# Kernel optimization log

Hardware: AMD Instinct MI355X
Metric: run time of the kernel (lower is better)

## Reference

```python
import jax, jax.numpy as jnp
import numpy as np

NS, NT, DIN, DOUT = 4096, 8192, 256, 128


def setup_inputs() -> dict:
    key = jax.random.key(0)
    k1, k2, k3, k4, k5, k6 = jax.random.split(key, 6)
    inp_s = jax.random.normal(k1, (NS, DIN), dtype=jnp.float32)
    inp_t = jax.random.normal(k2, (NT, DIN), dtype=jnp.float32)
    # nonnegative adjacency weights (original graphs have 0/1 entries)
    adj = jax.random.uniform(k3, (NS, NT), dtype=jnp.float32)
    adj_s = jax.random.uniform(k4, (NS, NS), dtype=jnp.float32)
    adj_t = jax.random.uniform(k5, (NT, NT), dtype=jnp.float32)
    init_range = np.sqrt(6.0 / (DIN + DOUT))
    W = jax.random.uniform(k6, (DIN, DOUT), minval=-init_range, maxval=init_range,
                           dtype=jnp.float32)
    return {"inp_s": inp_s, "inp_t": inp_t, "adj": adj, "adj_s": adj_s,
            "adj_t": adj_t, "W": W}


def reference(inp_s, inp_t, adj, adj_s, adj_t, W):
    # project both node sets with shared weights (dropout = 0.0)
    x = inp_s @ W                                   # [Ns, Dout]
    y = inp_t @ W                                   # [Nt, Dout]

    # degree normalization (add-one before sqrt)
    deg_so = jnp.sum(adj, axis=1, keepdims=True) + jnp.sum(adj_s, axis=1, keepdims=True)  # [Ns,1]
    root_deg_so = jnp.sqrt(deg_so + 1.0)            # [Ns,1]
    deg_to = jnp.sum(adj, axis=0, keepdims=True) + jnp.sum(adj_t, axis=0, keepdims=True)  # [1,Nt]
    root_deg_to = jnp.sqrt(deg_to + 1.0)            # [1,Nt]

    nrm_adj_s = adj_s / root_deg_so / root_deg_so.T  # [Ns,Ns]
    nrm_adj_t = adj_t / root_deg_to / root_deg_to.T  # [Nt,Nt]
    nrm_adj = adj / root_deg_so / root_deg_to        # [Ns,Nt]

    x = jax.nn.relu(x / root_deg_so + nrm_adj_s @ x + nrm_adj @ y)
    # note: updated (activated) x feeds into y's cross term, as in the original
    y = jax.nn.relu(y / root_deg_to.T + nrm_adj_t @ y + nrm_adj.T @ x)
    return (x, y)
```

## Files before the change

### kernel.cpp

```cpp
#include <hip/hip_runtime.h>

#define NS 4096
#define NT 8192
#define DIN 256
#define DOUT 128

#define OFF_RS   0
#define OFF_RT   (NS)
#define OFF_C1   (OFF_RT + NT)
#define OFF_C2   (OFF_C1 + NS*DOUT)
#define OFF_XS   (OFF_C2 + NT*DOUT)
#define OFF_YS   (OFF_XS + NS*DOUT)
#define OFF_XNS  (OFF_YS + NT*DOUT)
#define OFF_XST  (OFF_XNS + NS*DOUT)
#define OFF_YST  (OFF_XST + (128*NS)/2)

typedef __attribute__((ext_vector_type(8))) short bf8v;
typedef __attribute__((ext_vector_type(4))) float f32x4;
typedef __attribute__((ext_vector_type(4))) unsigned short u16x4;

__device__ __forceinline__ ushort f2bf(float f) {
    unsigned x = __float_as_uint(f);
    unsigned r = (x + 0x7fffu + ((x >> 16) & 1u)) >> 16;
    return (ushort)r;
}

__global__ void zero_kernel(float* __restrict__ p, int n4) {
    int i = blockIdx.x * blockDim.x + threadIdx.x;
    int stride = gridDim.x * blockDim.x;
    float4* p4 = (float4*)p;
    float4 z = make_float4(0.f, 0.f, 0.f, 0.f);
    for (; i < n4; i += stride) p4[i] = z;
}

__global__ __launch_bounds__(256)
void deg_mega_kernel(const float* __restrict__ adj,
                     const float* __restrict__ adj_s,
                     const float* __restrict__ adj_t,
                     float* __restrict__ deg_s, float* __restrict__ deg_t) {
    const int tid = threadIdx.x;
    const int lane = tid & 63;
    const int bid = blockIdx.x;
    if (bid < 1024) {
        const int c4 = (bid & 7) * 256 + tid;
        const int r0 = (bid >> 3) * 64;
        const float4* A4 = (const float4*)adj_t + (size_t)r0 * (NT / 4) + c4;
        float sx = 0.f, sy = 0.f, sz = 0.f, sw = 0.f;
#pragma unroll 8
        for (int r = 0; r < 64; ++r) {
            float4 v = A4[(size_t)r * (NT / 4)];
            sx += v.x; sy += v.y; sz += v.z; sw += v.w;
        }
        float* d = deg_t + c4 * 4;
        unsafeAtomicAdd(d + 0, sx);
        unsafeAtomicAdd(d + 1, sy);
        unsafeAtomicAdd(d + 2, sz);
        unsafeAtomicAdd(d + 3, sw);
    } else if (bid < 2048) {
        const int b = bid - 1024;
        const int c4 = (b & 7) * 256 + tid;
        const int r0 = (b >> 3) * 32;
        const float4* A4 = (const float4*)adj + (size_t)r0 * (NT / 4) + c4;
        float sx = 0.f, sy = 0.f, sz = 0.f, sw = 0.f;
#pragma unroll 8
        for (int r = 0; r < 32; ++r) {
            float4 v = A4[(size_t)r * (NT / 4)];
            sx += v.x; sy += v.y; sz += v.z; sw += v.w;
            float rp = v.x + v.y + v.z + v.w;
#pragma unroll
            for (int off = 32; off > 0; off >>= 1) rp += __shfl_down(rp, off, 64);
            if (lane == 0) unsafeAtomicAdd(deg_s + r0 + r, rp);
        }
        float* d = deg_t + c4 * 4;
        unsafeAtomicAdd(d + 0, sx);
        unsafeAtomicAdd(d + 1, sy);
        unsafeAtomicAdd(d + 2, sz);
        unsafeAtomicAdd(d + 3, sw);
    } else {
        const int b = bid - 2048;
        const int wid = tid >> 6;
        const int row = b * 4 + wid;
        const float4* p = (const float4*)(adj_s + (size_t)row * NS);
        float sum = 0.f;
#pragma unroll 8
        for (int c = lane; c < NS / 4; c += 64) { float4 v = p[c]; sum += v.x + v.y + v.z + v.w; }
#pragma unroll
        for (int off = 32; off > 0; off >>= 1) sum += __shfl_down(sum, off, 64);
        if (lane == 0) unsafeAtomicAdd(deg_s + row, sum);
    }
}

__global__ void finish_deg_kernel(float* __restrict__ deg) {
    int t = blockIdx.x * blockDim.x + threadIdx.x;
    deg[t] = sqrtf(deg[t] + 1.0f);
}

__global__ __launch_bounds__(256)
void proj_scale_kernel(const float* __restrict__ inp_s,
                       const float* __restrict__ inp_t,
                       const float* __restrict__ W,
                       const float* __restrict__ rs, const float* __restrict__ rt,
                       float* __restrict__ xs, float* __restrict__ ys,
                       ushort* __restrict__ xsT, ushort* __restrict__ ysT) {
    __shared__ float As[32][68];
    __shared__ float Bs[32][128];
    const int tid = threadIdx.x;

    const float* inp; const float* rdeg; float* outp; ushort* outT; int M; int m0;
    if (blockIdx.x < NS / 64) {
        inp = inp_s; rdeg = rs; outp = xs; outT = xsT; M = NS; m0 = blockIdx.x * 64;
    } else {
        int b = blockIdx.x - NS / 64;
        inp = inp_t; rdeg = rt; outp = ys; outT = ysT; M = NT; m0 = b * 64;
    }

    const int tx = tid & 15, ty = tid >> 4;
    const int arow = tid >> 3, acg = tid & 7;
    const int bk = tid >> 5, bng = tid & 31;

    float acc[4][8];
#pragma unroll
    for (int r = 0; r < 4; ++r)
#pragma unroll
        for (int c = 0; c < 8; ++c) acc[r][c] = 0.f;

    for (int kt = 0; kt < DIN; kt += 32) {
        const float* Ab = inp + (size_t)(m0 + arow) * DIN + kt + acg * 4;
        float4 a0 = *(const float4*)Ab;
        float4 a1 = *(const float4*)(Ab + (size_t)32 * DIN);
        const float* Bb = W + (size_t)(kt + bk) * DOUT + bng * 4;
        float4 b0 = *(const float4*)Bb;
        float4 b1 = *(const float4*)(Bb + 8 * DOUT);
        float4 b2 = *(const float4*)(Bb + 16 * DOUT);
        float4 b3 = *(const float4*)(Bb + 24 * DOUT);
        __syncthreads();
        As[acg * 4 + 0][arow] = a0.x;
        As[acg * 4 + 1][arow] = a0.y;
        As[acg * 4 + 2][arow] = a0.z;
        As[acg * 4 + 3][arow] = a0.w;
        As[acg * 4 + 0][arow + 32] = a1.x;
        As[acg * 4 + 1][arow + 32] = a1.y;
        As[acg * 4 + 2][arow + 32] = a1.z;
        As[acg * 4 + 3][arow + 32] = a1.w;
        *(float4*)&Bs[bk][bng * 4] = b0;
        *(float4*)&Bs[bk + 8][bng * 4] = b1;
        *(float4*)&Bs[bk + 16][bng * 4] = b2;
        *(float4*)&Bs[bk + 24][bng * 4] = b3;
        __syncthreads();
#pragma unroll
        for (int k = 0; k < 32; ++k) {
            float4 av = *(const float4*)&As[k][ty * 4];
            float4 bv0 = *(const float4*)&Bs[k][tx * 4];
            float4 bv1 = *(const float4*)&Bs[k][tx * 4 + 64];
            float a[4] = {av.x, av.y, av.z, av.w};
            float b[8] = {bv0.x, bv0.y, bv0.z, bv0.w, bv1.x, bv1.y, bv1.z, bv1.w};
#pragma unroll
            for (int r = 0; r < 4; ++r)
#pragma unroll
                for (int c = 0; c < 8; ++c) acc[r][c] = fmaf(a[r], b[c], acc[r][c]);
        }
    }
    float rds[4];
#pragma unroll
    for (int r = 0; r < 4; ++r) rds[r] = rdeg[m0 + ty * 4 + r];
#pragma unroll
    for (int r = 0; r < 4; ++r) {
        int row = m0 + ty * 4 + r;
        float* orow = outp + (size_t)row * DOUT;
#pragma unroll
        for (int c = 0; c < 8; ++c) acc[r][c] /= rds[r];
#pragma unroll
        for (int c = 0; c < 4; ++c) {
            orow[tx * 4 + c] = acc[r][c];
            orow[tx * 4 + 64 + c] = acc[r][4 + c];
        }
    }
#pragma unroll
    for (int c = 0; c < 8; ++c) {
        int col = tx * 4 + (c & 3) + (c >> 2) * 64;
        u16x4 w;
#pragma unroll
        for (int r = 0; r < 4; ++r) w[r] = f2bf(acc[r][c]);
        *(u16x4*)&outT[(size_t)col * M + m0 + ty * 4] = w;
    }
}

template<int TRANS, int BTF>
__device__ __forceinline__
void gemm_body(ushort (*As)[40], ushort (*Bs)[40],
               const float* __restrict__ A, int lda,
               const float* __restrict__ Bf,
               const ushort* __restrict__ bT, int ldb,
               float* __restrict__ C, int kchunk, int k0, int m0) {
    const int tid = threadIdx.x;
    const int lane = tid & 63, wid = tid >> 6;
    const int wm = (wid >> 1) * 64, wn = (wid & 1) * 64;
    const int r16 = lane & 15, kg = lane >> 4;

    const int s_kr = tid >> 3, s_f4 = tid & 7;
    const int a_r = tid >> 1, a_seg = tid & 1;
    const int t_n = tid >> 2, t_seg = tid & 3;

    f32x4 acc[4][4];
#pragma unroll
    for (int i = 0; i < 4; ++i)
#pragma unroll
        for (int j = 0; j < 4; ++j) acc[i][j] = (f32x4)(0.f);

    float4 aP[4], bP[4];
    bf8v bPT[2];

    auto loadB = [&](int ktb) {
        if (BTF) {
            const ushort* Tb = bT + (size_t)t_n * ldb + k0 + ktb + t_seg * 8;
            bPT[0] = *(const bf8v*)Tb;
            bPT[1] = *(const bf8v*)(Tb + (size_t)64 * ldb);
        } else {
            const float* Bb = Bf + (size_t)(k0 + ktb + s_kr) * DOUT + s_f4 * 4;
#pragma unroll
            for (int i = 0; i < 4; ++i) bP[i] = *(const float4*)(Bb + i * 32);
        }
    };
    auto loadA = [&](int ktb) {
        if (TRANS) {
            const float* Ab = A + (size_t)(k0 + ktb + s_kr) * lda + m0 + s_f4 * 4;
#pragma unroll
            for (int i = 0; i < 4; ++i) aP[i] = *(const float4*)(Ab + i * 32);
        } else {
            const float* Ab = A + (size_t)(m0 + a_r) * lda + k0 + ktb + a_seg * 16;
#pragma unroll
            for (int i = 0; i < 4; ++i) aP[i] = *(const float4*)(Ab + i * 4);
        }
    };

    loadB(0); loadA(0);

    for (int kt = 0; kt < kchunk; kt += 32) {
        __syncthreads();
        if (TRANS) {
#pragma unroll
            for (int i = 0; i < 4; ++i) {
                int m = s_f4 * 4 + i * 32;
                As[m + 0][s_kr] = f2bf(aP[i].x);
                As[m + 1][s_kr] = f2bf(aP[i].y);
                As[m + 2][s_kr] = f2bf(aP[i].z);
                As[m + 3][s_kr] = f2bf(aP[i].w);
            }
        } else {
            bf8v w0, w1;
            w0[0] = (short)f2bf(aP[0].x); w0[1] = (short)f2bf(aP[0].y);
            w0[2] = (short)f2bf(aP[0].z); w0[3] = (short)f2bf(aP[0].w);
            w0[4] = (short)f2bf(aP[1].x); w0[5] = (short)f2bf(aP[1].y);
            w0[6] = (short)f2bf(aP[1].z); w0[7] = (short)f2bf(aP[1].w);
            w1[0] = (short)f2bf(aP[2].x); w1[1] = (short)f2bf(aP[2].y);
            w1[2] = (short)f2bf(aP[2].z); w1[3] = (short)f2bf(aP[2].w);
            w1[4] = (short)f2bf(aP[3].x); w1[5] = (short)f2bf(aP[3].y);
            w1[6] = (short)f2bf(aP[3].z); w1[7] = (short)f2bf(aP[3].w);
            *(bf8v*)&As[a_r][a_seg * 16] = w0;
            *(bf8v*)&As[a_r][a_seg * 16 + 8] = w1;
        }
        if (BTF) {
            *(bf8v*)&Bs[t_n][t_seg * 8] = bPT[0];
            *(bf8v*)&Bs[t_n + 64][t_seg * 8] = bPT[1];
        } else {
#pragma unroll
            for (int i = 0; i < 4; ++i) {
                int n = s_f4 * 4 + i * 32;
                Bs[n + 0][s_kr] = f2bf(bP[i].x);
                Bs[n + 1][s_kr] = f2bf(bP[i].y);
                Bs[n + 2][s_kr] = f2bf(bP[i].z);
                Bs[n + 3][s_kr] = f2bf(bP[i].w);
            }
        }
        __syncthreads();

        if (kt + 32 < kchunk) { loadB(kt + 32); loadA(kt + 32); }

        bf8v af[4], bfv[4];
#pragma unroll
        for (int f = 0; f < 4; ++f) af[f] = *(const bf8v*)&As[wm + f * 16 + r16][kg * 8];
#pragma unroll
        for (int f = 0; f < 4; ++f) bfv[f] = *(const bf8v*)&Bs[wn + f * 16 + r16][kg * 8];
#pragma unroll
        for (int i = 0; i < 4; ++i)
#pragma unroll
            for (int j = 0; j < 4; ++j)
                acc[i][j] = __builtin_amdgcn_mfma_f32_16x16x32_bf16(af[i], bfv[j], acc[i][j], 0, 0, 0);
    }

    const int crow0 = m0 + wm + (lane >> 4) * 4;
#pragma unroll
    for (int i = 0; i < 4; ++i) {
#pragma unroll
        for (int j = 0; j < 4; ++j) {
            float* base = C + (size_t)(crow0 + i * 16) * DOUT + wn + j * 16 + r16;
            unsafeAtomicAdd(base + 0 * DOUT, acc[i][j][0]);
            unsafeAtomicAdd(base + 1 * DOUT, acc[i][j][1]);
            unsafeAtomicAdd(base + 2 * DOUT, acc[i][j][2]);
            unsafeAtomicAdd(base + 3 * DOUT, acc[i][j][3]);
        }
    }
}

__global__ __launch_bounds__(256)
void gemm_triple_kernel(const float* __restrict__ A0, int lda0, const ushort* __restrict__ B0T, int ldb0, int kc0, int n0,
                        const float* __restrict__ A1, int lda1, const ushort* __restrict__ B1T, int ldb1, int kc1, int n1,
                        const float* __restrict__ A2, int lda2, const ushort* __restrict__ B2T, int ldb2, int kc2,
                        float* __restrict__ C0, float* __restrict__ C2) {
    __shared__ ushort As[128][40];
    __shared__ ushort Bs[128][40];
    int bid = blockIdx.x;
    if (bid < n0) {
        gemm_body<0, 1>(As, Bs, A0, lda0, nullptr, B0T, ldb0, C0, kc0, (bid & 7) * kc0, (bid >> 3) * 128);
    } else if (bid < n0 + n1) {
        int b = bid - n0;
        gemm_body<0, 1>(As, Bs, A1, lda1, nullptr, B1T, ldb1, C0, kc1, (b & 7) * kc1, (b >> 3) * 128);
    } else {
        int b = bid - n0 - n1;
        gemm_body<0, 1>(As, Bs, A2, lda2, nullptr, B2T, ldb2, C2, kc2, (b & 7) * kc2, (b >> 3) * 128);
    }
}

template<int TRANS, int BTF>
__global__ __launch_bounds__(256)
void gemm_single_kernel(const float* __restrict__ A, int lda,
                        const float* __restrict__ Bf, const ushort* __restrict__ bT, int ldb,
                        float* __restrict__ C, int kchunk) {
    __shared__ ushort As[128][40];
    __shared__ ushort Bs[128][40];
    gemm_body<TRANS, BTF>(As, Bs, A, lda, Bf, bT, ldb, C, kchunk, blockIdx.y * kchunk, blockIdx.x * 128);
}

__global__ void epilogue1_kernel(const float* __restrict__ C1,
                                 const float* __restrict__ xs,
                                 const float* __restrict__ rs,
                                 float* __restrict__ outx,
                                 float* __restrict__ xns) {
    int idx = blockIdx.x * blockDim.x + threadIdx.x;
    if (idx >= NS * DOUT) return;
    int row = idx >> 7;
    float r = rs[row];
    float v = xs[idx] + C1[idx] / r;
    v = v > 0.f ? v : 0.f;
    outx[idx] = v;
    xns[idx] = v / r;
}

__global__ void epilogue2_kernel(const float* __restrict__ C2,
                                 const float* __restrict__ ys,
                                 const float* __restrict__ rt,
                                 float* __restrict__ outy) {
    int idx = blockIdx.x * blockDim.x + threadIdx.x;
    if (idx >= NT * DOUT) return;
    int row = idx >> 7;
    float v = ys[idx] + C2[idx] / rt[row];
    v = v > 0.f ? v : 0.f;
    outy[idx] = v;
}

extern "C" void kernel_launch(void* const* d_in, const int* in_sizes, int n_in,
                              void* d_out, int out_size, void* d_ws, size_t ws_size,
                              hipStream_t stream) {
    const float* inp_s = (const float*)d_in[0];
    const float* inp_t = (const float*)d_in[1];
    const float* adj   = (const float*)d_in[2];
    const float* adj_s = (const float*)d_in[3];
    const float* adj_t = (const float*)d_in[4];
    const float* W     = (const float*)d_in[5];
    float* out = (float*)d_out;
    float* ws  = (float*)d_ws;

    float* rs  = ws + OFF_RS;
    float* rt  = ws + OFF_RT;
    float* C1  = ws + OFF_C1;
    float* C2  = ws + OFF_C2;
    float* xs  = ws + OFF_XS;
    float* ys  = ws + OFF_YS;
    float* xns = ws + OFF_XNS;
    ushort* xsT = (ushort*)(ws + OFF_XST);
    ushort* ysT = (ushort*)(ws + OFF_YST);

    zero_kernel<<<1024, 256, 0, stream>>>(ws, OFF_XS / 4);

    deg_mega_kernel<<<3072, 256, 0, stream>>>(adj, adj_s, adj_t, rs, rt);
    finish_deg_kernel<<<(NS + NT) / 256, 256, 0, stream>>>(rs);

    proj_scale_kernel<<<(NS + NT) / 64, 256, 0, stream>>>(inp_s, inp_t, W, rs, rt, xs, ys, xsT, ysT);

    gemm_triple_kernel<<<1024, 256, 0, stream>>>(
        adj_s, NS, xsT, NS, NS / 8, 256,
        adj,   NT, ysT, NT, NT / 8, 256,
        adj_t, NT, ysT, NT, NT / 8,
        C1, C2);
    epilogue1_kernel<<<(NS * DOUT) / 256, 256, 0, stream>>>(C1, xs, rs, out, xns);

    gemm_single_kernel<1, 0><<<dim3(NT / 128, 8), 256, 0, stream>>>(adj, NT, xns, nullptr, 0, C2, NS / 8);
    epilogue2_kernel<<<(NT * DOUT) / 256, 256, 0, stream>>>(C2, ys, rt, out + NS * DOUT);
}
```

Baseline: 325.9 us.

## Replace atomic accumulation with per-split partial buffers reduced in epilogues

Split-K GEMM results and degree sums are no longer accumulated with float atomics into zeroed buffers. Each split writes its own partial slice, and the finish-degree and epilogue kernels sum the slices, vectorised with float4. This drops the zeroing kernel and the atomic contention, and makes the results deterministic. In exchange it adds extra memory traffic from writing and reading 16 partial C copies and a larger workspace, and the degree kernel now uses fewer, longer-running blocks.

```diff
diff --git a/kernel.cpp b/kernel.cpp
--- a/kernel.cpp
+++ b/kernel.cpp
@@ -7,9 +7,13 @@
 
 #define OFF_RS   0
 #define OFF_RT   (NS)
-#define OFF_C1   (OFF_RT + NT)
-#define OFF_C2   (OFF_C1 + NS*DOUT)
-#define OFF_XS   (OFF_C2 + NT*DOUT)
+#define OFF_RS0  (OFF_RT + NT)
+#define OFF_PROW (OFF_RS0 + NS)
+#define OFF_PTT  (OFF_PROW + 32*NS)
+#define OFF_PTA  (OFF_PTT + 32*NT)
+#define OFF_C1P  (OFF_PTA + 16*NT)
+#define OFF_C2P  (OFF_C1P + 16*NS*DOUT)
+#define OFF_XS   (OFF_C2P + 16*NT*DOUT)
 #define OFF_YS   (OFF_XS + NS*DOUT)
 #define OFF_XNS  (OFF_YS + NT*DOUT)
 #define OFF_XST  (OFF_XNS + NS*DOUT)
@@ -25,59 +29,46 @@
     return (ushort)r;
 }
 
-__global__ void zero_kernel(float* __restrict__ p, int n4) {
-    int i = blockIdx.x * blockDim.x + threadIdx.x;
-    int stride = gridDim.x * blockDim.x;
-    float4* p4 = (float4*)p;
-    float4 z = make_float4(0.f, 0.f, 0.f, 0.f);
-    for (; i < n4; i += stride) p4[i] = z;
-}
-
 __global__ __launch_bounds__(256)
 void deg_mega_kernel(const float* __restrict__ adj,
                      const float* __restrict__ adj_s,
                      const float* __restrict__ adj_t,
-                     float* __restrict__ deg_s, float* __restrict__ deg_t) {
+                     float* __restrict__ rs0, float* __restrict__ prow,
+                     float* __restrict__ ptt, float* __restrict__ pta) {
     const int tid = threadIdx.x;
     const int lane = tid & 63;
     const int bid = blockIdx.x;
-    if (bid < 1024) {
+    if (bid < 256) {
         const int c4 = (bid & 7) * 256 + tid;
-        const int r0 = (bid >> 3) * 64;
+        const int r0 = (bid >> 3) * 256;
         const float4* A4 = (const float4*)adj_t + (size_t)r0 * (NT / 4) + c4;
         float sx = 0.f, sy = 0.f, sz = 0.f, sw = 0.f;
 #pragma unroll 8
-        for (int r = 0; r < 64; ++r) {
+        for (int r = 0; r < 256; ++r) {
             float4 v = A4[(size_t)r * (NT / 4)];
             sx += v.x; sy += v.y; sz += v.z; sw += v.w;
         }
-        float* d = deg_t + c4 * 4;
-        unsafeAtomicAdd(d + 0, sx);
-        unsafeAtomicAdd(d + 1, sy);
-        unsafeAtomicAdd(d + 2, sz);
-        unsafeAtomicAdd(d + 3, sw);
-    } else if (bid < 2048) {
-        const int b = bid - 1024;
+        *(float4*)&ptt[(size_t)(bid >> 3) * NT + c4 * 4] = make_float4(sx, sy, sz, sw);
+    } else if (bid < 384) {
+        const int b = bid - 256;
         const int c4 = (b & 7) * 256 + tid;
-        const int r0 = (b >> 3) * 32;
+        const int r0 = (b >> 3) * 256;
+        const int wid = tid >> 6;
         const float4* A4 = (const float4*)adj + (size_t)r0 * (NT / 4) + c4;
+        float* prow_w = prow + (size_t)((b & 7) * 4 + wid) * NS;
         float sx = 0.f, sy = 0.f, sz = 0.f, sw = 0.f;
-#pragma unroll 8
-        for (int r = 0; r < 32; ++r) {
+#pragma unroll 4
+        for (int r = 0; r < 256; ++r) {
             float4 v = A4[(size_t)r * (NT / 4)];
             sx += v.x; sy += v.y; sz += v.z; sw += v.w;
             float rp = v.x + v.y + v.z + v.w;
 #pragma unroll
             for (int off = 32; off > 0; off >>= 1) rp += __shfl_down(rp, off, 64);
-            if (lane == 0) unsafeAtomicAdd(deg_s + r0 + r, rp);
-        }
-        float* d = deg_t + c4 * 4;
-        unsafeAtomicAdd(d + 0, sx);
-        unsafeAtomicAdd(d + 1, sy);
-        unsafeAtomicAdd(d + 2, sz);
-        unsafeAtomicAdd(d + 3, sw);
+            if (lane == 0) prow_w[r0 + r] = rp;
+        }
+        *(float4*)&pta[(size_t)(b >> 3) * NT + c4 * 4] = make_float4(sx, sy, sz, sw);
     } else {
-        const int b = bid - 2048;
+        const int b = bid - 384;
         const int wid = tid >> 6;
         const int row = b * 4 + wid;
         const float4* p = (const float4*)(adj_s + (size_t)row * NS);
@@ -86,13 +77,30 @@
         for (int c = lane; c < NS / 4; c += 64) { float4 v = p[c]; sum += v.x + v.y + v.z + v.w; }
 #pragma unroll
         for (int off = 32; off > 0; off >>= 1) sum += __shfl_down(sum, off, 64);
-        if (lane == 0) unsafeAtomicAdd(deg_s + row, sum);
-    }
-}
-
-__global__ void finish_deg_kernel(float* __restrict__ deg) {
+        if (lane == 0) rs0[row] = sum;
+    }
+}
+
+__global__ void finish_deg_kernel(const float* __restrict__ rs0,
+                                  const float* __restrict__ prow,
+                                  const float* __restrict__ ptt,
+                                  const float* __restrict__ pta,
+                                  float* __restrict__ rs, float* __restrict__ rt) {
     int t = blockIdx.x * blockDim.x + threadIdx.x;
-    deg[t] = sqrtf(deg[t] + 1.0f);
+    if (t < NS) {
+        float s = rs0[t];
+#pragma unroll
+        for (int i = 0; i < 32; ++i) s += prow[(size_t)i * NS + t];
+        rs[t] = sqrtf(s + 1.0f);
+    } else if (t < NS + NT) {
+        int c = t - NS;
+        float s = 0.f;
+#pragma unroll
+        for (int i = 0; i < 32; ++i) s += ptt[(size_t)i * NT + c];
+#pragma unroll
+        for (int i = 0; i < 16; ++i) s += pta[(size_t)i * NT + c];
+        rt[c] = sqrtf(s + 1.0f);
+    }
 }
 
 __global__ __launch_bounds__(256)
@@ -294,68 +302,94 @@
 #pragma unroll
         for (int j = 0; j < 4; ++j) {
             float* base = C + (size_t)(crow0 + i * 16) * DOUT + wn + j * 16 + r16;
-            unsafeAtomicAdd(base + 0 * DOUT, acc[i][j][0]);
-            unsafeAtomicAdd(base + 1 * DOUT, acc[i][j][1]);
-            unsafeAtomicAdd(base + 2 * DOUT, acc[i][j][2]);
-            unsafeAtomicAdd(base + 3 * DOUT, acc[i][j][3]);
+            base[0 * DOUT] = acc[i][j][0];
+            base[1 * DOUT] = acc[i][j][1];
+            base[2 * DOUT] = acc[i][j][2];
+            base[3 * DOUT] = acc[i][j][3];
         }
     }
 }
 
 __global__ __launch_bounds__(256)
-void gemm_triple_kernel(const float* __restrict__ A0, int lda0, const ushort* __restrict__ B0T, int ldb0, int kc0, int n0,
-                        const float* __restrict__ A1, int lda1, const ushort* __restrict__ B1T, int ldb1, int kc1, int n1,
-                        const float* __restrict__ A2, int lda2, const ushort* __restrict__ B2T, int ldb2, int kc2,
-                        float* __restrict__ C0, float* __restrict__ C2) {
+void gemm_triple_kernel(const float* __restrict__ adj_s,
+                        const float* __restrict__ adj,
+                        const float* __restrict__ adj_t,
+                        const ushort* __restrict__ xsT,
+                        const ushort* __restrict__ ysT,
+                        float* __restrict__ C1P, float* __restrict__ C2P) {
     __shared__ ushort As[128][40];
     __shared__ ushort Bs[128][40];
     int bid = blockIdx.x;
-    if (bid < n0) {
-        gemm_body<0, 1>(As, Bs, A0, lda0, nullptr, B0T, ldb0, C0, kc0, (bid & 7) * kc0, (bid >> 3) * 128);
-    } else if (bid < n0 + n1) {
-        int b = bid - n0;
-        gemm_body<0, 1>(As, Bs, A1, lda1, nullptr, B1T, ldb1, C0, kc1, (b & 7) * kc1, (b >> 3) * 128);
+    if (bid < 256) {
+        int s = bid & 7;
+        gemm_body<0, 1>(As, Bs, adj_s, NS, nullptr, xsT, NS,
+                        C1P + (size_t)s * (NS * DOUT), NS / 8, s * (NS / 8), (bid >> 3) * 128);
+    } else if (bid < 512) {
+        int b = bid - 256, s = b & 7;
+        gemm_body<0, 1>(As, Bs, adj, NT, nullptr, ysT, NT,
+                        C1P + (size_t)(8 + s) * (NS * DOUT), NT / 8, s * (NT / 8), (b >> 3) * 128);
     } else {
-        int b = bid - n0 - n1;
-        gemm_body<0, 1>(As, Bs, A2, lda2, nullptr, B2T, ldb2, C2, kc2, (b & 7) * kc2, (b >> 3) * 128);
-    }
-}
-
-template<int TRANS, int BTF>
+        int b = bid - 512, s = b & 7;
+        gemm_body<0, 1>(As, Bs, adj_t, NT, nullptr, ysT, NT,
+                        C2P + (size_t)s * (NT * DOUT), NT / 8, s * (NT / 8), (b >> 3) * 128);
+    }
+}
+
 __global__ __launch_bounds__(256)
-void gemm_single_kernel(const float* __restrict__ A, int lda,
-                        const float* __restrict__ Bf, const ushort* __restrict__ bT, int ldb,
-                        float* __restrict__ C, int kchunk) {
+void gemm_trans_kernel(const float* __restrict__ adj,
+                       const float* __restrict__ xns,
+                       float* __restrict__ C2P) {
     __shared__ ushort As[128][40];
     __shared__ ushort Bs[128][40];
-    gemm_body<TRANS, BTF>(As, Bs, A, lda, Bf, bT, ldb, C, kchunk, blockIdx.y * kchunk, blockIdx.x * 128);
-}
-
-__global__ void epilogue1_kernel(const float* __restrict__ C1,
+    int s = blockIdx.y;
+    gemm_body<1, 0>(As, Bs, adj, NT, xns, nullptr, 0,
+                    C2P + (size_t)(8 + s) * (NT * DOUT), NS / 8, s * (NS / 8), blockIdx.x * 128);
+}
+
+__global__ void epilogue1_kernel(const float* __restrict__ C1P,
                                  const float* __restrict__ xs,
                                  const float* __restrict__ rs,
                                  float* __restrict__ outx,
                                  float* __restrict__ xns) {
-    int idx = blockIdx.x * blockDim.x + threadIdx.x;
-    if (idx >= NS * DOUT) return;
-    int row = idx >> 7;
-    float r = rs[row];
-    float v = xs[idx] + C1[idx] / r;
-    v = v > 0.f ? v : 0.f;
-    outx[idx] = v;
-    xns[idx] = v / r;
-}
-
-__global__ void epilogue2_kernel(const float* __restrict__ C2,
+    int i4 = blockIdx.x * blockDim.x + threadIdx.x;
+    if (i4 >= NS * DOUT / 4) return;
+    float4 s = ((const float4*)C1P)[i4];
+#pragma unroll
+    for (int p = 1; p < 16; ++p) {
+        float4 v = ((const float4*)(C1P + (size_t)p * (NS * DOUT)))[i4];
+        s.x += v.x; s.y += v.y; s.z += v.z; s.w += v.w;
+    }
+    float r = rs[i4 >> 5];
+    float4 x = ((const float4*)xs)[i4];
+    float4 o, n;
+    o.x = fmaxf(x.x + s.x / r, 0.f); n.x = o.x / r;
+    o.y = fmaxf(x.y + s.y / r, 0.f); n.y = o.y / r;
+    o.z = fmaxf(x.z + s.z / r, 0.f); n.z = o.z / r;
+    o.w = fmaxf(x.w + s.w / r, 0.f); n.w = o.w / r;
+    ((float4*)outx)[i4] = o;
+    ((float4*)xns)[i4] = n;
+}
+
+__global__ void epilogue2_kernel(const float* __restrict__ C2P,
                                  const float* __restrict__ ys,
                                  const float* __restrict__ rt,
                                  float* __restrict__ outy) {
-    int idx = blockIdx.x * blockDim.x + threadIdx.x;
-    if (idx >= NT * DOUT) return;
-    int row = idx >> 7;
-    float v = ys[idx] + C2[idx] / rt[row];
-    v = v > 0.f ? v : 0.f;
-    outy[idx] = v;
+    int i4 = blockIdx.x * blockDim.x + threadIdx.x;
+    if (i4 >= NT * DOUT / 4) return;
+    float4 s = ((const float4*)C2P)[i4];
+#pragma unroll
+    for (int p = 1; p < 16; ++p) {
+        float4 v = ((const float4*)(C2P + (size_t)p * (NT * DOUT)))[i4];
+        s.x += v.x; s.y += v.y; s.z += v.z; s.w += v.w;
+    }
+    float r = rt[i4 >> 5];
+    float4 y = ((const float4*)ys)[i4];
+    float4 o;
+    o.x = fmaxf(y.x + s.x / r, 0.f);
+    o.y = fmaxf(y.y + s.y / r, 0.f);
+    o.z = fmaxf(y.z + s.z / r, 0.f);
+    o.w = fmaxf(y.w + s.w / r, 0.f);
+    ((float4*)outy)[i4] = o;
 }
 
 extern "C" void kernel_launch(void* const* d_in, const int* in_sizes, int n_in,
@@ -370,30 +404,28 @@
     float* out = (float*)d_out;
     float* ws  = (float*)d_ws;
 
-    float* rs  = ws + OFF_RS;
-    float* rt  = ws + OFF_RT;
-    float* C1  = ws + OFF_C1;
-    float* C2  = ws + OFF_C2;
-    float* xs  = ws + OFF_XS;
-    float* ys  = ws + OFF_YS;
-    float* xns = ws + OFF_XNS;
+    float* rs   = ws + OFF_RS;
+    float* rt   = ws + OFF_RT;
+    float* rs0  = ws + OFF_RS0;
+    float* prow = ws + OFF_PROW;
+    float* ptt  = ws + OFF_PTT;
+    float* pta  = ws + OFF_PTA;
+    float* C1P  = ws + OFF_C1P;
+    float* C2P  = ws + OFF_C2P;
+    float* xs   = ws + OFF_XS;
+    float* ys   = ws + OFF_YS;
+    float* xns  = ws + OFF_XNS;
     ushort* xsT = (ushort*)(ws + OFF_XST);
     ushort* ysT = (ushort*)(ws + OFF_YST);
 
-    zero_kernel<<<1024, 256, 0, stream>>>(ws, OFF_XS / 4);
-
-    deg_mega_kernel<<<3072, 256, 0, stream>>>(adj, adj_s, adj_t, rs, rt);
-    finish_deg_kernel<<<(NS + NT) / 256, 256, 0, stream>>>(rs);
+    deg_mega_kernel<<<1408, 256, 0, stream>>>(adj, adj_s, adj_t, rs0, prow, ptt, pta);
+    finish_deg_kernel<<<(NS + NT) / 256, 256, 0, stream>>>(rs0, prow, ptt, pta, rs, rt);
 
     proj_scale_kernel<<<(NS + NT) / 64, 256, 0, stream>>>(inp_s, inp_t, W, rs, rt, xs, ys, xsT, ysT);
 
-    gemm_triple_kernel<<<1024, 256, 0, stream>>>(
-        adj_s, NS, xsT, NS, NS / 8, 256,
-        adj,   NT, ysT, NT, NT / 8, 256,
-        adj_t, NT, ysT, NT, NT / 8,
-        C1, C2);
-    epilogue1_kernel<<<(NS * DOUT) / 256, 256, 0, stream>>>(C1, xs, rs, out, xns);
-
-    gemm_single_kernel<1, 0><<<dim3(NT / 128, 8), 256, 0, stream>>>(adj, NT, xns, nullptr, 0, C2, NS / 8);
-    epilogue2_kernel<<<(NT * DOUT) / 256, 256, 0, stream>>>(C2, ys, rt, out + NS * DOUT);
-}
+    gemm_triple_kernel<<<1024, 256, 0, stream>>>(adj_s, adj, adj_t, xsT, ysT, C1P, C2P);
+    epilogue1_kernel<<<(NS * DOUT / 4 + 255) / 256, 256, 0, stream>>>(C1P, xs, rs, out, xns);
+
+    gemm_trans_kernel<<<dim3(NT / 128, 8), 256, 0, stream>>>(adj, xns, C2P);
+    epilogue2_kernel<<<(NT * DOUT / 4 + 255) / 256, 256, 0, stream>>>(C2P, ys, rt, out + NS * DOUT);
+}
```

New measurement: 412.9 us. 1.27x slower.
